# Kernel optimization log

Measured on AMD Instinct MI355X. Metric: run time of the kernel, lower is better.

The kernel has to match this reference:

```python
import jax, jax.numpy as jnp
import numpy as np

B, L, DIM = 1, 2048, 512
DHEAD = 64
HEADS = DIM // DHEAD  # 8
KS = 127              # kernel_size (odd)
EXP = 4


def setup_inputs() -> dict:
    key = jax.random.key(0)
    ks = jax.random.split(key, 8)
    sc = 0.02
    rnd = lambda k, shape: (jax.random.normal(k, shape, jnp.float32) * sc)
    return {
        "x": jax.random.normal(ks[0], (B, L, DIM), jnp.float32),
        "ln1_g": jnp.ones((DIM,), jnp.float32),
        "ln1_b": jnp.zeros((DIM,), jnp.float32),
        "qkv_w": rnd(ks[1], (DIM, 3 * DIM)),
        "qkv_b": jnp.zeros((3 * DIM,), jnp.float32),
        "rpb": rnd(ks[2], (HEADS, 2 * KS - 1)),
        "proj_w": rnd(ks[3], (DIM, DIM)),
        "proj_b": jnp.zeros((DIM,), jnp.float32),
        "ln2_g": jnp.ones((DIM,), jnp.float32),
        "ln2_b": jnp.zeros((DIM,), jnp.float32),
        "ff1_w": rnd(ks[4], (DIM, DIM * EXP)),
        "ff1_b": jnp.zeros((DIM * EXP,), jnp.float32),
        "ff2_w": rnd(ks[5], (DIM * EXP, DIM)),
        "ff2_b": jnp.zeros((DIM,), jnp.float32),
    }


def _layernorm(x, g, b, eps=1e-5):
    m = x.mean(-1, keepdims=True)
    v = ((x - m) ** 2).mean(-1, keepdims=True)
    return (x - m) * jax.lax.rsqrt(v + eps) * g + b


def _neighborhood_attn_1d(x, qkv_w, qkv_b, rpb, proj_w, proj_b):
    # NATTEN NeighborhoodAttention1D: window of KS keys per query, clamped
    # at sequence edges so every query sees exactly KS keys (requires L >= KS).
    b, l, dim = x.shape
    qkv = (x @ qkv_w + qkv_b).reshape(b, l, 3, HEADS, DHEAD)
    q, k, v = qkv[:, :, 0], qkv[:, :, 1], qkv[:, :, 2]  # [b,l,h,d]
    scale = DHEAD ** -0.5
    # window start per query, clamped to stay in-bounds
    starts = jnp.clip(jnp.arange(l) - KS // 2, 0, l - KS)          # [l]
    idx = starts[:, None] + jnp.arange(KS)                         # [l,KS]
    kg = k[:, idx]                                                 # [b,l,KS,h,d]
    vg = v[:, idx]                                                 # [b,l,KS,h,d]
    logits = jnp.einsum('blhd,blkhd->blhk', q * scale, kg)         # [b,l,h,KS]
    # relative-position bias: index = (j - i) + (KS - 1), in [0, 2KS-2]
    bias_idx = idx - jnp.arange(l)[:, None] + (KS - 1)             # [l,KS]
    logits = logits + rpb[:, bias_idx].transpose(1, 0, 2)[None]    # [1,l,h,KS]
    attn = jax.nn.softmax(logits, axis=-1)
    out = jnp.einsum('blhk,blkhd->blhd', attn, vg).reshape(b, l, dim)
    return out @ proj_w + proj_b


def reference(x, ln1_g, ln1_b, qkv_w, qkv_b, rpb, proj_w, proj_b,
              ln2_g, ln2_b, ff1_w, ff1_b, ff2_w, ff2_b):
    x = x + _neighborhood_attn_1d(_layernorm(x, ln1_g, ln1_b),
                                  qkv_w, qkv_b, rpb, proj_w, proj_b)
    h = _layernorm(x, ln2_g, ln2_b)
    h = jax.nn.gelu(h @ ff1_w + ff1_b, approximate=False) @ ff2_w + ff2_b
    return x + h
```

## Files before the change

kernel.cpp:

```cpp
#include <hip/hip_runtime.h>
#include <hip/hip_bf16.h>

static constexpr int Lc     = 2048;
static constexpr int DIMc   = 512;
static constexpr int HEADSc = 8;
static constexpr int DHEADc = 64;
static constexpr int KSc    = 127;
static constexpr int NQKVc  = 1536;

typedef __attribute__((ext_vector_type(8))) short short8;
typedef __attribute__((ext_vector_type(4))) float f32x4;
typedef unsigned short u16;
typedef unsigned int u32;

__device__ __forceinline__ float b2f(u16 s) {
  return __uint_as_float(((u32)s) << 16);
}
__device__ __forceinline__ u16 f2b(float x) {
  u32 u = __float_as_uint(x);
  return (u16)((u + 0x7fffu + ((u >> 16) & 1u)) >> 16);
}
__device__ __forceinline__ void gload16(const void* g, void* l) {
  __builtin_amdgcn_global_load_lds(
      (const __attribute__((address_space(1))) u32*)g,
      (__attribute__((address_space(3))) u32*)l, 16, 0, 0);
}

__global__ __launch_bounds__(256) void prep_kernel(
    const float* __restrict__ w0, const float* __restrict__ w1,
    const float* __restrict__ w2, const float* __restrict__ w3,
    u16* __restrict__ o0, u16* __restrict__ o1, u16* __restrict__ o2,
    u16* __restrict__ o3, const float* __restrict__ xin,
    const float* __restrict__ g, const float* __restrict__ b,
    u16* __restrict__ lnout) {
  __shared__ float tl[32][33];
  __shared__ float rs[4], rq[4], stat[2];
  const int tid = threadIdx.x;
  if (blockIdx.x >= 3072) {
    const int row = blockIdx.x - 3072;
    const float* rp = xin + (size_t)row * DIMc;
    float v0 = rp[tid];
    float v1 = rp[tid + 256];
    float s = v0 + v1;
    float sq = v0 * v0 + v1 * v1;
#pragma unroll
    for (int o = 32; o > 0; o >>= 1) {
      s += __shfl_down(s, o);
      sq += __shfl_down(sq, o);
    }
    const int wid = tid >> 6, lane = tid & 63;
    if (lane == 0) { rs[wid] = s; rq[wid] = sq; }
    __syncthreads();
    if (tid == 0) {
      float S = rs[0] + rs[1] + rs[2] + rs[3];
      float Q = rq[0] + rq[1] + rq[2] + rq[3];
      float m = S / DIMc;
      float var = Q / DIMc - m * m;
      stat[0] = m;
      stat[1] = rsqrtf(var + 1e-5f);
    }
    __syncthreads();
    const float m = stat[0], r = stat[1];
    lnout[(size_t)row * DIMc + tid] = f2b((v0 - m) * r * g[tid] + b[tid]);
    lnout[(size_t)row * DIMc + tid + 256] =
        f2b((v1 - m) * r * g[tid + 256] + b[tid + 256]);
    return;
  }
  int t = blockIdx.x;
  const float* W;
  u16* O;
  int K, N;
  if (t < 768)       { W = w0; O = o0; K = 512;  N = 1536; }
  else if (t < 1024) { W = w1; O = o1; K = 512;  N = 512;  t -= 768; }
  else if (t < 2048) { W = w2; O = o2; K = 512;  N = 2048; t -= 1024; }
  else               { W = w3; O = o3; K = 2048; N = 512;  t -= 2048; }
  const int nt = N >> 5;
  const int by = t / nt, bx = t % nt;
  const int c = tid & 31, r0 = tid >> 5;
#pragma unroll
  for (int i = 0; i < 4; ++i) {
    const int r = r0 + i * 8;
    tl[r][c] = W[(size_t)(by * 32 + r) * N + bx * 32 + c];
  }
  __syncthreads();
#pragma unroll
  for (int i = 0; i < 4; ++i) {
    const int r = r0 + i * 8;
    O[(size_t)(bx * 32 + r) * K + by * 32 + c] = f2b(tl[c][r]);
  }
}

__global__ __launch_bounds__(256) void ln2_kernel(const float* __restrict__ in,
                                                  const float* __restrict__ g,
                                                  const float* __restrict__ b,
                                                  u16* __restrict__ out) {
  const int row = blockIdx.x;
  const int tid = threadIdx.x;
  const float* rp = in + (size_t)row * DIMc;
  float v0 = rp[tid];
  float v1 = rp[tid + 256];
  float s = v0 + v1;
  float sq = v0 * v0 + v1 * v1;
  __shared__ float rs[4], rq[4], stat[2];
#pragma unroll
  for (int o = 32; o > 0; o >>= 1) {
    s += __shfl_down(s, o);
    sq += __shfl_down(sq, o);
  }
  const int wid = tid >> 6, lane = tid & 63;
  if (lane == 0) { rs[wid] = s; rq[wid] = sq; }
  __syncthreads();
  if (tid == 0) {
    float S = rs[0] + rs[1] + rs[2] + rs[3];
    float Q = rq[0] + rq[1] + rq[2] + rq[3];
    float m = S / DIMc;
    float var = Q / DIMc - m * m;
    stat[0] = m;
    stat[1] = rsqrtf(var + 1e-5f);
  }
  __syncthreads();
  const float m = stat[0], r = stat[1];
  out[(size_t)row * DIMc + tid] = f2b((v0 - m) * r * g[tid] + b[tid]);
  out[(size_t)row * DIMc + tid + 256] =
      f2b((v1 - m) * r * g[tid + 256] + b[tid + 256]);
}

template <int OP, typename OUT_T>
__global__ __launch_bounds__(128) void mfma_gemm(
    const u16* __restrict__ A, const u16* __restrict__ Bt,
    const float* __restrict__ bias, const float* __restrict__ res,
    OUT_T* __restrict__ C, int M, int N, int K) {
  constexpr int BK = 64;
  __shared__ __align__(16) u16 As[2][64 * BK];
  __shared__ __align__(16) u16 Bs[2][64 * BK];
  const int tid = threadIdx.x;
  const int wave = tid >> 6, lane = tid & 63;
  const int m0 = blockIdx.y * 64, n0 = blockIdx.x * 64;
  const int wn = wave * 32;
  const int T = K / BK;

  f32x4 acc[4][2] = {};

  const int fr = lane & 15;
  const int hi = lane >> 4;

  const int lrow = wave * 8 + (lane >> 3);
  const int lcol = ((lane & 7) ^ (lane >> 3)) * 8;

#define STAGE(k0, buf)                                                        \
  {                                                                           \
    _Pragma("unroll") for (int p = 0; p < 4; ++p) {                           \
      gload16(A + (size_t)(m0 + p * 16 + lrow) * K + (k0) + lcol,             \
              &As[buf][p * 1024 + wave * 512]);                               \
      gload16(Bt + (size_t)(n0 + p * 16 + lrow) * K + (k0) + lcol,            \
              &Bs[buf][p * 1024 + wave * 512]);                               \
    }                                                                         \
  }

  STAGE(0, 0);
  STAGE(BK, 1);

  for (int t = 0; t < T; ++t) {
    const int cur = t & 1;
    if (t + 1 < T) {
      asm volatile("s_waitcnt vmcnt(8)" ::: "memory");
    } else {
      asm volatile("s_waitcnt vmcnt(0)" ::: "memory");
    }
    __builtin_amdgcn_s_barrier();

    short8 af[4][2], bf[2][2];
#pragma unroll
    for (int i = 0; i < 4; ++i) {
      const int row = i * 16 + fr;
      const char* rb = (const char*)As[cur] + row * 128;
#pragma unroll
      for (int ks = 0; ks < 2; ++ks)
        af[i][ks] =
            *(const short8*)(rb + ((ks * 64 + hi * 16) ^ ((fr & 7) << 4)));
    }
#pragma unroll
    for (int j = 0; j < 2; ++j) {
      const int row = wn + j * 16 + fr;
      const char* rb = (const char*)Bs[cur] + row * 128;
#pragma unroll
      for (int ks = 0; ks < 2; ++ks)
        bf[j][ks] =
            *(const short8*)(rb + ((ks * 64 + hi * 16) ^ ((fr & 7) << 4)));
    }
    asm volatile("s_waitcnt lgkmcnt(0)" ::: "memory");
    __builtin_amdgcn_sched_barrier(0);
    __builtin_amdgcn_s_barrier();

    if (t + 2 < T) STAGE((t + 2) * BK, cur);

#pragma unroll
    for (int ks = 0; ks < 2; ++ks)
#pragma unroll
      for (int i = 0; i < 4; ++i)
#pragma unroll
        for (int j = 0; j < 2; ++j)
          acc[i][j] = __builtin_amdgcn_mfma_f32_16x16x32_bf16(
              af[i][ks], bf[j][ks], acc[i][j], 0, 0, 0);
  }
#undef STAGE

  const int cl = lane & 15;
  const int rbase = (lane >> 4) * 4;
#pragma unroll
  for (int i = 0; i < 4; ++i) {
#pragma unroll
    for (int j = 0; j < 2; ++j) {
      const int c = n0 + wn + j * 16 + cl;
      const float bv = bias[c];
#pragma unroll
      for (int r = 0; r < 4; ++r) {
        const int row = m0 + i * 16 + rbase + r;
        float v = acc[i][j][r] + bv;
        if (OP == 1) v = 0.5f * v * (1.0f + erff(v * 0.70710678118f));
        const size_t o = (size_t)row * N + c;
        if (OP == 2) {
          ((float*)C)[o] = v + res[o];
        } else {
          ((u16*)C)[o] = f2b(v);
        }
      }
    }
  }
}

__global__ __launch_bounds__(256) void attn_mfma(const u16* __restrict__ qkv,
                                                 const float* __restrict__ rpb,
                                                 u16* __restrict__ out) {
  constexpr int NR = 192, NT = 12, PP = 200;
  __shared__ __align__(16) u16 Ks[NR * DHEADc];
  __shared__ __align__(16) u16 Vt[DHEADc * NR];
  __shared__ __align__(16) u16 Ps[4][16 * PP];
  __shared__ float rp[2 * KSc - 1];
  const int h = blockIdx.y, l0 = blockIdx.x * 64, tid = threadIdx.x;
  const int wv = tid >> 6, lane = tid & 63;
  const int fr = lane & 15, hi = lane >> 4;

  int s_min = l0 - 63;
  if (s_min < 0) s_min = 0;
  if (s_min > Lc - KSc) s_min = Lc - KSc;

  for (int i = tid; i < 2 * KSc - 1; i += 256) rp[i] = rpb[h * (2 * KSc - 1) + i];

#pragma unroll
  for (int rd = 0; rd < 6; ++rd) {
    const int linear = rd * 4096 + wv * 1024 + lane * 16;
    const int row = linear >> 7;
    const int seg = (linear >> 4) & 7;
    const int segp = seg ^ (row & 7);
    int gl = s_min + row;
    if (gl > Lc - 1) gl = Lc - 1;
    gload16(qkv + (size_t)gl * NQKVc + DIMc + h * DHEADc + segp * 8,
            (char*)Ks + rd * 4096 + wv * 1024);
  }

#pragma unroll
  for (int rd = 0; rd < 3; ++rd) {
    const int t = rd * 256 + tid;
    const int rpair = t >> 3, seg = t & 7;
    const int r0 = rpair * 2;
    int g0 = s_min + r0, g1 = s_min + r0 + 1;
    if (g0 > Lc - 1) g0 = Lc - 1;
    if (g1 > Lc - 1) g1 = Lc - 1;
    const short8 a =
        *(const short8*)(qkv + (size_t)g0 * NQKVc + 2 * DIMc + h * DHEADc + seg * 8);
    const short8 bq =
        *(const short8*)(qkv + (size_t)g1 * NQKVc + 2 * DIMc + h * DHEADc + seg * 8);
#pragma unroll
    for (int j = 0; j < 8; ++j) {
      const int d = seg * 8 + j;
      int byte = d * (NR * 2) + r0 * 2;
      byte ^= (d & 7) << 4;
      *(u32*)((char*)Vt + byte) =
          ((u32)(u16)a[j]) | (((u32)(u16)bq[j]) << 16);
    }
  }

  const int lq = l0 + wv * 16 + fr;
  short8 qf[2];
#pragma unroll
  for (int ks = 0; ks < 2; ++ks)
    qf[ks] = *(const short8*)(qkv + (size_t)lq * NQKVc + h * DHEADc + ks * 32 + hi * 8);

  __syncthreads();

  f32x4 S[NT] = {};
#pragma unroll
  for (int jt = 0; jt < NT; ++jt) {
#pragma unroll
    for (int ks = 0; ks < 2; ++ks) {
      int byte = (jt * 16 + fr) * 128 + ks * 64 + hi * 16;
      byte ^= (fr & 7) << 4;
      const short8 kf = *(const short8*)((const char*)Ks + byte);
      S[jt] = __builtin_amdgcn_mfma_f32_16x16x32_bf16(qf[ks], kf, S[jt], 0, 0, 0);
    }
  }

  float inv4[4];
#pragma unroll
  for (int r = 0; r < 4; ++r) {
    const int l = l0 + wv * 16 + hi * 4 + r;
    int st = l - 63;
    if (st < 0) st = 0;
    if (st > Lc - KSc) st = Lc - KSc;
    float mx = -3e38f;
#pragma unroll
    for (int jt = 0; jt < NT; ++jt) {
      const int pos = s_min + jt * 16 + fr;
      const int j = pos - st;
      float v = -3e38f;
      if (j >= 0 && j <= KSc - 1) v = S[jt][r] * 0.125f + rp[pos - l + KSc - 1];
      S[jt][r] = v;
      mx = fmaxf(mx, v);
    }
#pragma unroll
    for (int o = 1; o < 16; o <<= 1) mx = fmaxf(mx, __shfl_xor(mx, o));
    float sum = 0.f;
#pragma unroll
    for (int jt = 0; jt < NT; ++jt) {
      const float e = __expf(S[jt][r] - mx);
      S[jt][r] = e;
      sum += e;
    }
#pragma unroll
    for (int o = 1; o < 16; o <<= 1) sum += __shfl_xor(sum, o);
    inv4[r] = 1.f / sum;
  }

#pragma unroll
  for (int jt = 0; jt < NT; ++jt)
#pragma unroll
    for (int r = 0; r < 4; ++r)
      Ps[wv][(hi * 4 + r) * PP + jt * 16 + fr] = f2b(S[jt][r] * inv4[r]);

  f32x4 O[4] = {};
#pragma unroll
  for (int ks = 0; ks < 6; ++ks) {
    const short8 pa =
        *(const short8*)((const char*)Ps[wv] + fr * (PP * 2) + ks * 64 + hi * 16);
#pragma unroll
    for (int dt = 0; dt < 4; ++dt) {
      int byte = (dt * 16 + fr) * (NR * 2) + ks * 64 + hi * 16;
      byte ^= (fr & 7) << 4;
      const short8 vb = *(const short8*)((const char*)Vt + byte);
      O[dt] = __builtin_amdgcn_mfma_f32_16x16x32_bf16(pa, vb, O[dt], 0, 0, 0);
    }
  }

#pragma unroll
  for (int dt = 0; dt < 4; ++dt)
#pragma unroll
    for (int r = 0; r < 4; ++r)
      out[(size_t)(l0 + wv * 16 + hi * 4 + r) * DIMc + h * DHEADc + dt * 16 + fr] =
          f2b(O[dt][r]);
}

extern "C" void kernel_launch(void* const* d_in, const int* in_sizes, int n_in,
                              void* d_out, int out_size, void* d_ws,
                              size_t ws_size, hipStream_t stream) {
  const float* x      = (const float*)d_in[0];
  const float* ln1_g  = (const float*)d_in[1];
  const float* ln1_b  = (const float*)d_in[2];
  const float* qkv_w  = (const float*)d_in[3];
  const float* qkv_b  = (const float*)d_in[4];
  const float* rpb    = (const float*)d_in[5];
  const float* proj_w = (const float*)d_in[6];
  const float* proj_b = (const float*)d_in[7];
  const float* ln2_g  = (const float*)d_in[8];
  const float* ln2_b  = (const float*)d_in[9];
  const float* ff1_w  = (const float*)d_in[10];
  const float* ff1_b  = (const float*)d_in[11];
  const float* ff2_w  = (const float*)d_in[12];
  const float* ff2_b  = (const float*)d_in[13];
  float* out = (float*)d_out;

  char* ws = (char*)d_ws;
  u16*   lnbuf   = (u16*)(ws);
  u16*   qkvbuf  = (u16*)(ws + ((size_t)2  << 20));
  u16*   attnbuf = (u16*)(ws + ((size_t)8  << 20));
  float* x2      = (float*)(ws + ((size_t)10 << 20));
  u16*   ff1buf  = (u16*)(ws + ((size_t)14 << 20));
  u16*   wt_qkv  = (u16*)(ws + ((size_t)22 << 20));
  u16*   wt_proj = (u16*)(ws + ((size_t)23 << 20) + ((size_t)512 << 10));
  u16*   wt_ff1  = (u16*)(ws + ((size_t)24 << 20));
  u16*   wt_ff2  = (u16*)(ws + ((size_t)26 << 20));

  prep_kernel<<<5120, 256, 0, stream>>>(qkv_w, proj_w, ff1_w, ff2_w, wt_qkv,
                                        wt_proj, wt_ff1, wt_ff2, x, ln1_g,
                                        ln1_b, lnbuf);
  mfma_gemm<0, u16><<<dim3(NQKVc / 64, Lc / 64), 128, 0, stream>>>(
      lnbuf, wt_qkv, qkv_b, nullptr, qkvbuf, Lc, NQKVc, DIMc);
  attn_mfma<<<dim3(Lc / 64, HEADSc), 256, 0, stream>>>(qkvbuf, rpb, attnbuf);
  mfma_gemm<2, float><<<dim3(DIMc / 64, Lc / 64), 128, 0, stream>>>(
      attnbuf, wt_proj, proj_b, x, x2, Lc, DIMc, DIMc);
  ln2_kernel<<<Lc, 256, 0, stream>>>(x2, ln2_g, ln2_b, lnbuf);
  mfma_gemm<1, u16><<<dim3(4 * DIMc / 64, Lc / 64), 128, 0, stream>>>(
      lnbuf, wt_ff1, ff1_b, nullptr, ff1buf, Lc, 4 * DIMc, DIMc);
  mfma_gemm<2, float><<<dim3(DIMc / 64, Lc / 64), 128, 0, stream>>>(
      ff1buf, wt_ff2, ff2_b, x2, out, Lc, DIMc, 4 * DIMc);
}
```

Before: 72.84 us.

## Run each 64x64 GEMM tile on a single wave and drop block barriers

The GEMM kernel now launches one 64-thread wave per 64x64 output tile instead of two waves each covering half the columns. That wave stages all A/B tiles itself, computes a 4x4 grid of MFMA accumulators, and the s_barrier calls around LDS reads are removed because only one wave touches the shared buffers. This trades intra-block parallelism (half the waves per CU for the same grid, twice the accumulators and loads per wave) for no barrier synchronisation and more operand reuse per wave. Latency hiding may suffer because fewer waves are resident, and the fourth launch-bounds argument also limits occupancy hints.

```diff
diff --git a/kernel.cpp b/kernel.cpp
--- a/kernel.cpp
+++ b/kernel.cpp
@@ -126,34 +126,33 @@
 }
 
 template <int OP, typename OUT_T>
-__global__ __launch_bounds__(128) void mfma_gemm(
+__global__ __launch_bounds__(64, 1) void mfma_gemm(
     const u16* __restrict__ A, const u16* __restrict__ Bt,
     const float* __restrict__ bias, const float* __restrict__ res,
     OUT_T* __restrict__ C, int M, int N, int K) {
   constexpr int BK = 64;
   __shared__ __align__(16) u16 As[2][64 * BK];
   __shared__ __align__(16) u16 Bs[2][64 * BK];
-  const int tid = threadIdx.x;
-  const int wave = tid >> 6, lane = tid & 63;
+  const int lane = threadIdx.x;
   const int m0 = blockIdx.y * 64, n0 = blockIdx.x * 64;
-  const int wn = wave * 32;
   const int T = K / BK;
 
-  f32x4 acc[4][2] = {};
+  f32x4 acc[4][4] = {};
 
   const int fr = lane & 15;
   const int hi = lane >> 4;
-
-  const int lrow = wave * 8 + (lane >> 3);
+  const int xr = (fr & 7) << 4;
+
+  const int lrow = lane >> 3;
   const int lcol = ((lane & 7) ^ (lane >> 3)) * 8;
 
 #define STAGE(k0, buf)                                                        \
   {                                                                           \
-    _Pragma("unroll") for (int p = 0; p < 4; ++p) {                           \
-      gload16(A + (size_t)(m0 + p * 16 + lrow) * K + (k0) + lcol,             \
-              &As[buf][p * 1024 + wave * 512]);                               \
-      gload16(Bt + (size_t)(n0 + p * 16 + lrow) * K + (k0) + lcol,            \
-              &Bs[buf][p * 1024 + wave * 512]);                               \
+    _Pragma("unroll") for (int p = 0; p < 8; ++p) {                           \
+      gload16(A + (size_t)(m0 + p * 8 + lrow) * K + (k0) + lcol,              \
+              &As[buf][p * 512]);                                             \
+      gload16(Bt + (size_t)(n0 + p * 8 + lrow) * K + (k0) + lcol,             \
+              &Bs[buf][p * 512]);                                             \
     }                                                                         \
   }
 
@@ -163,34 +162,26 @@
   for (int t = 0; t < T; ++t) {
     const int cur = t & 1;
     if (t + 1 < T) {
-      asm volatile("s_waitcnt vmcnt(8)" ::: "memory");
+      asm volatile("s_waitcnt vmcnt(16)" ::: "memory");
     } else {
       asm volatile("s_waitcnt vmcnt(0)" ::: "memory");
     }
-    __builtin_amdgcn_s_barrier();
-
-    short8 af[4][2], bf[2][2];
+
+    short8 af[4][2], bf[4][2];
 #pragma unroll
     for (int i = 0; i < 4; ++i) {
-      const int row = i * 16 + fr;
-      const char* rb = (const char*)As[cur] + row * 128;
-#pragma unroll
-      for (int ks = 0; ks < 2; ++ks)
-        af[i][ks] =
-            *(const short8*)(rb + ((ks * 64 + hi * 16) ^ ((fr & 7) << 4)));
-    }
-#pragma unroll
-    for (int j = 0; j < 2; ++j) {
-      const int row = wn + j * 16 + fr;
-      const char* rb = (const char*)Bs[cur] + row * 128;
-#pragma unroll
-      for (int ks = 0; ks < 2; ++ks)
-        bf[j][ks] =
-            *(const short8*)(rb + ((ks * 64 + hi * 16) ^ ((fr & 7) << 4)));
+      const char* rb = (const char*)As[cur] + (i * 16 + fr) * 128;
+      af[i][0] = *(const short8*)(rb + ((hi * 16) ^ xr));
+      af[i][1] = *(const short8*)(rb + ((64 + hi * 16) ^ xr));
+    }
+#pragma unroll
+    for (int j = 0; j < 4; ++j) {
+      const char* rb = (const char*)Bs[cur] + (j * 16 + fr) * 128;
+      bf[j][0] = *(const short8*)(rb + ((hi * 16) ^ xr));
+      bf[j][1] = *(const short8*)(rb + ((64 + hi * 16) ^ xr));
     }
     asm volatile("s_waitcnt lgkmcnt(0)" ::: "memory");
     __builtin_amdgcn_sched_barrier(0);
-    __builtin_amdgcn_s_barrier();
 
     if (t + 2 < T) STAGE((t + 2) * BK, cur);
 
@@ -199,7 +190,7 @@
 #pragma unroll
       for (int i = 0; i < 4; ++i)
 #pragma unroll
-        for (int j = 0; j < 2; ++j)
+        for (int j = 0; j < 4; ++j)
           acc[i][j] = __builtin_amdgcn_mfma_f32_16x16x32_bf16(
               af[i][ks], bf[j][ks], acc[i][j], 0, 0, 0);
   }
@@ -210,8 +201,8 @@
 #pragma unroll
   for (int i = 0; i < 4; ++i) {
 #pragma unroll
-    for (int j = 0; j < 2; ++j) {
-      const int c = n0 + wn + j * 16 + cl;
+    for (int j = 0; j < 4; ++j) {
+      const int c = n0 + j * 16 + cl;
       const float bv = bias[c];
 #pragma unroll
       for (int r = 0; r < 4; ++r) {
@@ -393,14 +384,14 @@
   prep_kernel<<<5120, 256, 0, stream>>>(qkv_w, proj_w, ff1_w, ff2_w, wt_qkv,
                                         wt_proj, wt_ff1, wt_ff2, x, ln1_g,
                                         ln1_b, lnbuf);
-  mfma_gemm<0, u16><<<dim3(NQKVc / 64, Lc / 64), 128, 0, stream>>>(
+  mfma_gemm<0, u16><<<dim3(NQKVc / 64, Lc / 64), 64, 0, stream>>>(
       lnbuf, wt_qkv, qkv_b, nullptr, qkvbuf, Lc, NQKVc, DIMc);
   attn_mfma<<<dim3(Lc / 64, HEADSc), 256, 0, stream>>>(qkvbuf, rpb, attnbuf);
-  mfma_gemm<2, float><<<dim3(DIMc / 64, Lc / 64), 128, 0, stream>>>(
+  mfma_gemm<2, float><<<dim3(DIMc / 64, Lc / 64), 64, 0, stream>>>(
       attnbuf, wt_proj, proj_b, x, x2, Lc, DIMc, DIMc);
   ln2_kernel<<<Lc, 256, 0, stream>>>(x2, ln2_g, ln2_b, lnbuf);
-  mfma_gemm<1, u16><<<dim3(4 * DIMc / 64, Lc / 64), 128, 0, stream>>>(
+  mfma_gemm<1, u16><<<dim3(4 * DIMc / 64, Lc / 64), 64, 0, stream>>>(
       lnbuf, wt_ff1, ff1_b, nullptr, ff1buf, Lc, 4 * DIMc, DIMc);
-  mfma_gemm<2, float><<<dim3(DIMc / 64, Lc / 64), 128, 0, stream>>>(
+  mfma_gemm<2, float><<<dim3(DIMc / 64, Lc / 64), 64, 0, stream>>>(
       ff1buf, wt_ff2, ff2_b, x2, out, Lc, DIMc, 4 * DIMc);
 }
```

Measured after the change: 76.81 us. +5.4%, slower.

## Add intra-block split-K GEMM for the proj and ff2 residual projections

Applied to the files above, without the earlier changes.

Adds a split-K GEMM kernel in which each of four waves takes a quarter of K with its own double-buffered LDS staging. Partial accumulators are reduced through shared memory, then bias and residual are added with vectorized fp32 stores. It replaces the older 128-thread kernel for the two N=512 GEMMs, which launched only 256 blocks, to get more waves per block and more latency hiding on the long-K ff2 GEMM. The cost is 64KB of LDS per block, limiting occupancy, plus an extra reduction pass.

```diff
diff --git a/kernel.cpp b/kernel.cpp
--- a/kernel.cpp
+++ b/kernel.cpp
@@ -218,14 +218,103 @@
         const int row = m0 + i * 16 + rbase + r;
         float v = acc[i][j][r] + bv;
         if (OP == 1) v = 0.5f * v * (1.0f + erff(v * 0.70710678118f));
-        const size_t o = (size_t)row * N + c;
-        if (OP == 2) {
-          ((float*)C)[o] = v + res[o];
-        } else {
-          ((u16*)C)[o] = f2b(v);
-        }
+        ((u16*)C)[(size_t)row * N + c] = f2b(v);
       }
     }
+  }
+}
+
+__global__ __launch_bounds__(256, 1) void mfma_gemm_ks(
+    const u16* __restrict__ A, const u16* __restrict__ Bt,
+    const float* __restrict__ bias, const float* __restrict__ res,
+    float* __restrict__ C, int M, int N, int K) {
+  constexpr int BK = 32;
+  __shared__ __align__(16) char LB[65536];
+  const int tid = threadIdx.x;
+  const int wave = tid >> 6, lane = tid & 63;
+  const int m0 = blockIdx.y * 64, n0 = blockIdx.x * 64;
+  const int kslice = K >> 2;
+  const int kbeg = wave * kslice;
+  const int T = kslice / BK;
+  char* myb = LB + wave * 16384;
+
+  f32x4 acc[4][4] = {};
+  const int fr = lane & 15;
+  const int hi = lane >> 4;
+
+  const int lrow = lane >> 2;
+  const int lcol = ((lane & 3) ^ ((lane >> 2) & 3)) * 8;
+
+#define KSTAGE(k0, b)                                                         \
+  {                                                                           \
+    _Pragma("unroll") for (int p = 0; p < 4; ++p) {                           \
+      gload16(A + (size_t)(m0 + p * 16 + lrow) * K + (k0) + lcol,             \
+              myb + (b) * 8192 + p * 1024);                                   \
+      gload16(Bt + (size_t)(n0 + p * 16 + lrow) * K + (k0) + lcol,            \
+              myb + (b) * 8192 + 4096 + p * 1024);                            \
+    }                                                                         \
+  }
+
+  KSTAGE(kbeg, 0);
+  KSTAGE(kbeg + BK, 1);
+
+  for (int t = 0; t < T; ++t) {
+    const int cur = t & 1;
+    if (t + 1 < T) {
+      asm volatile("s_waitcnt vmcnt(8)" ::: "memory");
+    } else {
+      asm volatile("s_waitcnt vmcnt(0)" ::: "memory");
+    }
+
+    short8 af[4], bf[4];
+#pragma unroll
+    for (int i = 0; i < 4; ++i) {
+      const char* rb = myb + cur * 8192 + (i * 16 + fr) * 64;
+      af[i] = *(const short8*)(rb + ((hi * 16) ^ ((fr & 3) << 4)));
+    }
+#pragma unroll
+    for (int j = 0; j < 4; ++j) {
+      const char* rb = myb + cur * 8192 + 4096 + (j * 16 + fr) * 64;
+      bf[j] = *(const short8*)(rb + ((hi * 16) ^ ((fr & 3) << 4)));
+    }
+    asm volatile("s_waitcnt lgkmcnt(0)" ::: "memory");
+    __builtin_amdgcn_sched_barrier(0);
+
+    if (t + 2 < T) KSTAGE(kbeg + (t + 2) * BK, cur);
+
+#pragma unroll
+    for (int i = 0; i < 4; ++i)
+#pragma unroll
+      for (int j = 0; j < 4; ++j)
+        acc[i][j] = __builtin_amdgcn_mfma_f32_16x16x32_bf16(af[i], bf[j],
+                                                            acc[i][j], 0, 0, 0);
+  }
+#undef KSTAGE
+
+  __syncthreads();
+  float* red = (float*)LB;
+  const int rbase = hi * 4;
+#pragma unroll
+  for (int i = 0; i < 4; ++i)
+#pragma unroll
+    for (int j = 0; j < 4; ++j)
+#pragma unroll
+      for (int r = 0; r < 4; ++r)
+        red[wave * 4096 + (i * 16 + rbase + r) * 64 + j * 16 + fr] =
+            acc[i][j][r];
+  __syncthreads();
+#pragma unroll
+  for (int q = 0; q < 4; ++q) {
+    const int idx = q * 1024 + tid * 4;
+    const int row = idx >> 6, col = idx & 63;
+    f32x4 s = *(const f32x4*)&red[idx];
+#pragma unroll
+    for (int w = 1; w < 4; ++w) s += *(const f32x4*)&red[w * 4096 + idx];
+    const f32x4 bb = *(const f32x4*)&bias[n0 + col];
+    const size_t o = (size_t)(m0 + row) * N + n0 + col;
+    const f32x4 rr = *(const f32x4*)&res[o];
+    s += bb + rr;
+    *(f32x4*)&C[o] = s;
   }
 }
 
@@ -396,11 +485,11 @@
   mfma_gemm<0, u16><<<dim3(NQKVc / 64, Lc / 64), 128, 0, stream>>>(
       lnbuf, wt_qkv, qkv_b, nullptr, qkvbuf, Lc, NQKVc, DIMc);
   attn_mfma<<<dim3(Lc / 64, HEADSc), 256, 0, stream>>>(qkvbuf, rpb, attnbuf);
-  mfma_gemm<2, float><<<dim3(DIMc / 64, Lc / 64), 128, 0, stream>>>(
+  mfma_gemm_ks<<<dim3(DIMc / 64, Lc / 64), 256, 0, stream>>>(
       attnbuf, wt_proj, proj_b, x, x2, Lc, DIMc, DIMc);
   ln2_kernel<<<Lc, 256, 0, stream>>>(x2, ln2_g, ln2_b, lnbuf);
   mfma_gemm<1, u16><<<dim3(4 * DIMc / 64, Lc / 64), 128, 0, stream>>>(
       lnbuf, wt_ff1, ff1_b, nullptr, ff1buf, Lc, 4 * DIMc, DIMc);
-  mfma_gemm<2, float><<<dim3(DIMc / 64, Lc / 64), 128, 0, stream>>>(
+  mfma_gemm_ks<<<dim3(DIMc / 64, Lc / 64), 256, 0, stream>>>(
       ff1buf, wt_ff2, ff2_b, x2, out, Lc, DIMc, 4 * DIMc);
 }
```

Result: faster. 68.06 us (-6.6%).
